# Kernel optimization log

Hardware: AMD Instinct MI355X
Metric: run time of the kernel (lower is better)

Reference implementation:

```python
import jax, jax.numpy as jnp
import numpy as np

EMBED_DIM = 768
N_HEADS = 12
HEAD_DIM = EMBED_DIM // N_HEADS
B, S = 8, 1024


def setup_inputs() -> dict:
    key = jax.random.key(0)
    ks = jax.random.split(key, 7)
    sc = 1.0 / np.sqrt(HEAD_DIM)
    return {
        "sequences": jax.random.normal(ks[0], (B, S, EMBED_DIM), dtype=jnp.float32),
        # per-head Linear weights stored [H, in, out] (torch Linear is x @ W.T + b;
        # with random init the layout convention is equivalent math)
        "Wq": jax.random.normal(ks[1], (N_HEADS, HEAD_DIM, HEAD_DIM), dtype=jnp.float32) * sc,
        "bq": jax.random.normal(ks[2], (N_HEADS, HEAD_DIM), dtype=jnp.float32) * 0.01,
        "Wk": jax.random.normal(ks[3], (N_HEADS, HEAD_DIM, HEAD_DIM), dtype=jnp.float32) * sc,
        "bk": jax.random.normal(ks[4], (N_HEADS, HEAD_DIM), dtype=jnp.float32) * 0.01,
        "Wv": jax.random.normal(ks[5], (N_HEADS, HEAD_DIM, HEAD_DIM), dtype=jnp.float32) * sc,
        "bv": jax.random.normal(ks[6], (N_HEADS, HEAD_DIM), dtype=jnp.float32) * 0.01,
    }


def reference(sequences, Wq, bq, Wk, bk, Wv, bv):
    b, s, d = sequences.shape
    h, hd = Wq.shape[0], Wq.shape[1]
    x = sequences.reshape(b, s, h, hd)              # split embed dim into heads
    q = jnp.einsum("bshd,hde->bshe", x, Wq) + bq    # per-head linear (block-diag GEMM)
    k = jnp.einsum("bshd,hde->bshe", x, Wk) + bk
    v = jnp.einsum("bshd,hde->bshe", x, Wv) + bv
    # NOTE: original module applies NO 1/sqrt(head_dim) scaling
    logits = jnp.einsum("bshe,bthe->bhst", q, k)    # [B,H,S,S]
    attn = jax.nn.softmax(logits, axis=-1)
    out = jnp.einsum("bhst,bthe->bshe", attn, v)    # [B,S,H,hd]
    return out.reshape(b, s, d)
```

## Files before the change

### kernel.cpp

```cpp
#include <hip/hip_runtime.h>
#include <stdint.h>

#define EMBED 768
#define NH 12
#define HD 64
#define Bsz 8
#define Ssz 1024
#define LOG2E 1.44269504088896f

typedef __attribute__((ext_vector_type(4))) float f32x4;
typedef __attribute__((ext_vector_type(8))) _Float16 f16x8;
typedef __attribute__((ext_vector_type(4))) _Float16 f16x4;
typedef __attribute__((ext_vector_type(2))) _Float16 f16x2;

__device__ __forceinline__ int SW(int row, int col) {
    return row * 64 + (col ^ ((row & 7) << 3));
}

__launch_bounds__(256)
__global__ void qkv_proj(const float* __restrict__ x,
                         const float* __restrict__ Wq, const float* __restrict__ bq,
                         const float* __restrict__ Wk, const float* __restrict__ bk,
                         const float* __restrict__ Wv, const float* __restrict__ bv,
                         _Float16* __restrict__ Qb, _Float16* __restrict__ Kb,
                         _Float16* __restrict__ Vt)
{
    __shared__ _Float16 XT[128 * 72];
    __shared__ _Float16 Wt[3 * 64 * 72];
    __shared__ float Bs[192];

    const int bt = blockIdx.x;
    const int st = bt & 7;
    const int h  = (bt >> 3) % NH;
    const int b  = bt / (8 * NH);
    const int sbase = st * 128;
    const int tid = threadIdx.x;
    const int lane = tid & 63, w = tid >> 6;
    const int l15 = lane & 15, quad = lane >> 4;

    for (int i = 0; i < 8; ++i) {
        int idx = tid + 256 * i;
        int row = idx >> 4;
        int c4  = (idx & 15) * 4;
        const float4 g = *(const float4*)&x[(size_t)(b * Ssz + sbase + row) * EMBED + h * HD + c4];
        f16x4 v; v[0] = (_Float16)g.x; v[1] = (_Float16)g.y; v[2] = (_Float16)g.z; v[3] = (_Float16)g.w;
        *(f16x4*)&XT[row * 72 + c4] = v;
    }
    {
        const float* Ws0[3] = {Wq, Wk, Wv};
        const float* bs0[3] = {bq, bk, bv};
#pragma unroll
        for (int m = 0; m < 3; ++m) {
            const float* W = Ws0[m] + (size_t)h * HD * HD;
            for (int i = 0; i < 4; ++i) {
                int idx = tid + 256 * i;
                int d = idx >> 4, e4 = (idx & 15) * 4;
                float4 g = *(const float4*)&W[d * 64 + e4];
                Wt[m * 4608 + (e4 + 0) * 72 + d] = (_Float16)g.x;
                Wt[m * 4608 + (e4 + 1) * 72 + d] = (_Float16)g.y;
                Wt[m * 4608 + (e4 + 2) * 72 + d] = (_Float16)g.z;
                Wt[m * 4608 + (e4 + 3) * 72 + d] = (_Float16)g.w;
            }
        }
        if (tid < 192) Bs[tid] = bs0[tid >> 6][h * HD + (tid & 63)];
    }
    __syncthreads();

    f16x8 bx[2][2];
    const int nbg0 = w * 2;
#pragma unroll
    for (int nb = 0; nb < 2; ++nb)
#pragma unroll
        for (int kh = 0; kh < 2; ++kh)
            bx[nb][kh] = *(const f16x8*)&XT[((nbg0 + nb) * 16 + l15) * 72 + kh * 32 + quad * 8];
    __syncthreads();

    const size_t qkbase = (size_t)(b * NH + h) * Ssz + sbase;
    const f32x4 zero = {0.f, 0.f, 0.f, 0.f};

#pragma unroll
    for (int m = 0; m < 3; ++m) {
        f32x4 acc[2][4];
#pragma unroll
        for (int nb = 0; nb < 2; ++nb)
#pragma unroll
            for (int eb = 0; eb < 4; ++eb) acc[nb][eb] = zero;
#pragma unroll
        for (int eb = 0; eb < 4; ++eb)
#pragma unroll
            for (int kh = 0; kh < 2; ++kh) {
                f16x8 aw = *(const f16x8*)&Wt[m * 4608 + (eb * 16 + l15) * 72 + kh * 32 + quad * 8];
#pragma unroll
                for (int nb = 0; nb < 2; ++nb)
                    acc[nb][eb] = __builtin_amdgcn_mfma_f32_16x16x32_f16(aw, bx[nb][kh], acc[nb][eb], 0, 0, 0);
            }

        if (m < 2) {
            const float sc = (m == 0) ? LOG2E : 1.0f;
#pragma unroll
            for (int nb = 0; nb < 2; ++nb)
#pragma unroll
                for (int eb = 0; eb < 4; ++eb) {
                    f32x4 bb = *(const f32x4*)&Bs[m * 64 + eb * 16 + quad * 4];
                    f16x4 v;
#pragma unroll
                    for (int r = 0; r < 4; ++r) v[r] = (_Float16)((acc[nb][eb][r] + bb[r]) * sc);
                    *(f16x4*)&XT[((nbg0 + nb) * 16 + l15) * 72 + eb * 16 + quad * 4] = v;
                }
            __syncthreads();
            _Float16* outp = (m == 0) ? Qb : Kb;
            for (int i = 0; i < 4; ++i) {
                int idx = tid + 256 * i;
                int s = idx >> 3, e8 = (idx & 7) * 8;
                *(f16x8*)&outp[(qkbase + s) * HD + e8] = *(const f16x8*)&XT[s * 72 + e8];
            }
            __syncthreads();
        } else {
            _Float16* Vs = XT;
#pragma unroll
            for (int nb = 0; nb < 2; ++nb)
#pragma unroll
                for (int eb = 0; eb < 4; ++eb) {
                    f32x4 bb = *(const f32x4*)&Bs[128 + eb * 16 + quad * 4];
#pragma unroll
                    for (int r = 0; r < 4; ++r)
                        Vs[(eb * 16 + quad * 4 + r) * 136 + (nbg0 + nb) * 16 + l15] =
                            (_Float16)(acc[nb][eb][r] + bb[r]);
                }
            __syncthreads();
            for (int i = 0; i < 4; ++i) {
                int idx = tid + 256 * i;
                int e = idx >> 4, s8 = (idx & 15) * 8;
                *(f16x8*)&Vt[((size_t)(b * NH + h) * 64 + e) * Ssz + sbase + s8] =
                    *(const f16x8*)&Vs[e * 136 + s8];
            }
        }
    }
}

#define KVBUF 9216
__launch_bounds__(512)
__global__ void attn(const _Float16* __restrict__ Qb, const _Float16* __restrict__ Kb,
                     const _Float16* __restrict__ Vt, float* __restrict__ out)
{
    __shared__ _Float16 KV[2 * KVBUF];
    __shared__ _Float16 Pl[8 * 16 * 64];

    const int bt = blockIdx.x;
    const int hh = bt % 96;
    const int qt = bt / 96;
    const int h  = hh % NH;
    const int b  = hh / NH;

    const int tid = threadIdx.x;
    const int lane = tid & 63, w = tid >> 6;
    const int l15 = lane & 15, quad = lane >> 4;

    const size_t bh = (size_t)(b * NH + h);
    const _Float16* Qg = Qb + bh * Ssz * HD;
    const _Float16* Kg = Kb + bh * Ssz * HD;
    const _Float16* Vg = Vt + bh * (size_t)HD * Ssz;

    const int qrow0 = qt * 128 + w * 16;
    f16x8 aq[2];
#pragma unroll
    for (int kh = 0; kh < 2; ++kh)
        aq[kh] = *(const f16x8*)&Qg[(qrow0 + l15) * HD + kh * 32 + quad * 8];

    const f32x4 zero = {0.f, 0.f, 0.f, 0.f};
    f32x4 o[5];
#pragma unroll
    for (int eb = 0; eb < 5; ++eb) o[eb] = zero;
    float m_run = -INFINITY;

    const int srow = tid >> 3;
    const int scol = (tid & 7) * 8;
    const int swst = SW(srow, scol);

    {
        int bufi = tid >> 8;
        int r16  = (tid >> 4) & 15;
        int c4   = (tid & 15) * 4;
        f16x4 v;
        _Float16 val = (r16 == 0) ? (_Float16)1.0f : (_Float16)0.0f;
        v[0] = val; v[1] = val; v[2] = val; v[3] = val;
        *(f16x4*)&KV[bufi * KVBUF + 4096 + SW(64 + r16, c4)] = v;
    }

    f16x8 kr = *(const f16x8*)&Kg[srow * HD + scol];
    f16x8 vr = *(const f16x8*)&Vg[(size_t)srow * Ssz + scol];
    *(f16x8*)&KV[swst] = kr;
    *(f16x8*)&KV[4096 + swst] = vr;
    __syncthreads();

    _Float16* Pw = &Pl[w * 1024];
    const int swq = (l15 & 7) << 3;

    for (int kt = 0; kt < 16; ++kt) {
        const int cur = kt & 1;
        if (kt < 15) {
            kr = *(const f16x8*)&Kg[((kt + 1) * 64 + srow) * HD + scol];
            vr = *(const f16x8*)&Vg[(size_t)srow * Ssz + (kt + 1) * 64 + scol];
        }
        const _Float16* Ksb = &KV[cur * KVBUF];
        const _Float16* Vsb = &KV[cur * KVBUF + 4096];

        f32x4 st[4];
#pragma unroll
        for (int tb = 0; tb < 4; ++tb) {
            f32x4 acc = zero;
#pragma unroll
            for (int kh = 0; kh < 2; ++kh) {
                f16x8 ak = *(const f16x8*)&Ksb[SW(tb * 16 + l15, kh * 32 + quad * 8)];
                acc = __builtin_amdgcn_mfma_f32_16x16x32_f16(ak, aq[kh], acc, 0, 0, 0);
            }
            st[tb] = acc;
        }

        float mt = st[0][0];
#pragma unroll
        for (int tb = 0; tb < 4; ++tb)
#pragma unroll
            for (int r = 0; r < 4; ++r) mt = fmaxf(mt, st[tb][r]);
        mt = fmaxf(mt, __shfl_xor(mt, 16, 64));
        mt = fmaxf(mt, __shfl_xor(mt, 32, 64));
        float mn = fmaxf(m_run, mt);
        float al = __builtin_amdgcn_exp2f(m_run - mn);
        m_run = mn;
        f16x4 pv[4];
#pragma unroll
        for (int tb = 0; tb < 4; ++tb) {
            float p0 = __builtin_amdgcn_exp2f(st[tb][0] - mn);
            float p1 = __builtin_amdgcn_exp2f(st[tb][1] - mn);
            float p2 = __builtin_amdgcn_exp2f(st[tb][2] - mn);
            float p3 = __builtin_amdgcn_exp2f(st[tb][3] - mn);
            f16x2 lo = __builtin_bit_cast(f16x2, __builtin_amdgcn_cvt_pkrtz(p0, p1));
            f16x2 hi = __builtin_bit_cast(f16x2, __builtin_amdgcn_cvt_pkrtz(p2, p3));
            pv[tb][0] = lo[0]; pv[tb][1] = lo[1]; pv[tb][2] = hi[0]; pv[tb][3] = hi[1];
        }

#pragma unroll
        for (int tb = 0; tb < 4; ++tb)
            *(f16x4*)&Pw[l15 * 64 + ((tb * 16 + quad * 4) ^ swq)] = pv[tb];

        if (kt < 15) {
            const int nxt = cur ^ 1;
            *(f16x8*)&KV[nxt * KVBUF + swst] = kr;
            *(f16x8*)&KV[nxt * KVBUF + 4096 + swst] = vr;
        }
        __asm__ __volatile__("s_waitcnt lgkmcnt(0)" ::: "memory");
        f16x8 bp[2];
#pragma unroll
        for (int kh = 0; kh < 2; ++kh)
            bp[kh] = *(const f16x8*)&Pw[l15 * 64 + ((kh * 32 + quad * 8) ^ swq)];

#pragma unroll
        for (int eb = 0; eb < 5; ++eb) o[eb] *= al;

#pragma unroll
        for (int kh = 0; kh < 2; ++kh)
#pragma unroll
            for (int eb = 0; eb < 5; ++eb) {
                f16x8 av = *(const f16x8*)&Vsb[SW(eb * 16 + l15, kh * 32 + quad * 8)];
                o[eb] = __builtin_amdgcn_mfma_f32_16x16x32_f16(av, bp[kh], o[eb], 0, 0, 0);
            }

        __syncthreads();
    }

    const float lv = __shfl(o[4][0], l15, 64);
    const float inv = 1.f / lv;
    const int q = qrow0 + l15;
    float* op = &out[(size_t)(b * Ssz + q) * EMBED + h * HD + quad * 4];
#pragma unroll
    for (int eb = 0; eb < 4; ++eb) {
        f32x4 r = o[eb] * inv;
        *(f32x4*)&op[eb * 16] = r;
    }
}

extern "C" void kernel_launch(void* const* d_in, const int* in_sizes, int n_in,
                              void* d_out, int out_size, void* d_ws, size_t ws_size,
                              hipStream_t stream) {
    const float* x  = (const float*)d_in[0];
    const float* Wq = (const float*)d_in[1];
    const float* bq = (const float*)d_in[2];
    const float* Wk = (const float*)d_in[3];
    const float* bk = (const float*)d_in[4];
    const float* Wv = (const float*)d_in[5];
    const float* bv = (const float*)d_in[6];

    _Float16* Qb = (_Float16*)d_ws;
    _Float16* Kb = Qb + (size_t)Bsz * NH * Ssz * HD;
    _Float16* Vt = Kb + (size_t)Bsz * NH * Ssz * HD;

    qkv_proj<<<dim3(Bsz * NH * 8), dim3(256), 0, stream>>>(x, Wq, bq, Wk, bk, Wv, bv, Qb, Kb, Vt);
    attn<<<dim3(Bsz * NH * 8), dim3(512), 0, stream>>>(Qb, Kb, Vt, (float*)d_out);
}
```

Baseline: 135.9 us.

## Restructure attention kernel around 32x32 MFMA with register-resident P and async LDS loads

Rewrites the attention kernel to use 32x32x16 MFMA tiles with 4 waves of 32 query rows each instead of 8 waves of 16 rows. The P tile now stays in registers, rearranged with cross-lane shuffles, instead of round-tripping through LDS. K/V tiles are staged with global_load_lds direct-to-LDS copies using pre-swizzled source addresses. The row sum is tracked explicitly instead of through the ones-row trick, rescaling is skipped unless the max grows by more than a threshold, and setprio hints wrap the MFMA sections. Fewer threads per block and the lazy rescale carry occupancy and numerical-range risks.

```diff
diff --git a/kernel.cpp b/kernel.cpp
--- a/kernel.cpp
+++ b/kernel.cpp
@@ -9,13 +9,11 @@
 #define LOG2E 1.44269504088896f
 
 typedef __attribute__((ext_vector_type(4))) float f32x4;
+typedef __attribute__((ext_vector_type(16))) float f32x16;
 typedef __attribute__((ext_vector_type(8))) _Float16 f16x8;
 typedef __attribute__((ext_vector_type(4))) _Float16 f16x4;
 typedef __attribute__((ext_vector_type(2))) _Float16 f16x2;
-
-__device__ __forceinline__ int SW(int row, int col) {
-    return row * 64 + (col ^ ((row & 7) << 3));
-}
+typedef __attribute__((ext_vector_type(4))) unsigned int u32x4;
 
 __launch_bounds__(256)
 __global__ void qkv_proj(const float* __restrict__ x,
@@ -138,13 +136,12 @@
     }
 }
 
-#define KVBUF 9216
-__launch_bounds__(512)
+#define KVB 8192
+__launch_bounds__(256)
 __global__ void attn(const _Float16* __restrict__ Qb, const _Float16* __restrict__ Kb,
                      const _Float16* __restrict__ Vt, float* __restrict__ out)
 {
-    __shared__ _Float16 KV[2 * KVBUF];
-    __shared__ _Float16 Pl[8 * 16 * 64];
+    __shared__ _Float16 KV[2 * KVB];
 
     const int bt = blockIdx.x;
     const int hh = bt % 96;
@@ -152,131 +149,157 @@
     const int h  = hh % NH;
     const int b  = hh / NH;
 
-    const int tid = threadIdx.x;
+    const int tid  = threadIdx.x;
     const int lane = tid & 63, w = tid >> 6;
-    const int l15 = lane & 15, quad = lane >> 4;
+    const int l31  = lane & 31;
+    const int hf   = lane >> 5;
+    const bool hi  = (hf != 0);
 
     const size_t bh = (size_t)(b * NH + h);
     const _Float16* Qg = Qb + bh * Ssz * HD;
     const _Float16* Kg = Kb + bh * Ssz * HD;
     const _Float16* Vg = Vt + bh * (size_t)HD * Ssz;
 
-    const int qrow0 = qt * 128 + w * 16;
-    f16x8 aq[2];
-#pragma unroll
-    for (int kh = 0; kh < 2; ++kh)
-        aq[kh] = *(const f16x8*)&Qg[(qrow0 + l15) * HD + kh * 32 + quad * 8];
-
-    const f32x4 zero = {0.f, 0.f, 0.f, 0.f};
-    f32x4 o[5];
-#pragma unroll
-    for (int eb = 0; eb < 5; ++eb) o[eb] = zero;
-    float m_run = -INFINITY;
-
-    const int srow = tid >> 3;
-    const int scol = (tid & 7) * 8;
-    const int swst = SW(srow, scol);
-
-    {
-        int bufi = tid >> 8;
-        int r16  = (tid >> 4) & 15;
-        int c4   = (tid & 15) * 4;
-        f16x4 v;
-        _Float16 val = (r16 == 0) ? (_Float16)1.0f : (_Float16)0.0f;
-        v[0] = val; v[1] = val; v[2] = val; v[3] = val;
-        *(f16x4*)&KV[bufi * KVBUF + 4096 + SW(64 + r16, c4)] = v;
-    }
-
-    f16x8 kr = *(const f16x8*)&Kg[srow * HD + scol];
-    f16x8 vr = *(const f16x8*)&Vg[(size_t)srow * Ssz + scol];
-    *(f16x8*)&KV[swst] = kr;
-    *(f16x8*)&KV[4096 + swst] = vr;
+    const int qrow = qt * 128 + w * 32 + l31;
+    f16x8 aq[4];
+#pragma unroll
+    for (int kk = 0; kk < 4; ++kk)
+        aq[kk] = *(const f16x8*)&Qg[(size_t)qrow * HD + kk * 16 + hf * 8];
+
+    const int ca = tid, cb = tid + 256;
+    const int ra = ca >> 3, ga = (ca & 7) ^ (ra & 7);
+    const int rb = cb >> 3, gb = (cb & 7) ^ (rb & 7);
+    const _Float16* Ka  = Kg + ra * HD + ga * 8;
+    const _Float16* Kb2 = Kg + rb * HD + gb * 8;
+    const _Float16* Va  = Vg + (size_t)ra * Ssz + ga * 8;
+    const _Float16* Vb  = Vg + (size_t)rb * Ssz + gb * 8;
+
+#define STAGE(buf, kt_) do {                                                            \
+    __builtin_amdgcn_global_load_lds(                                                   \
+        (const __attribute__((address_space(1))) void*)(Ka + (kt_) * 64 * HD),          \
+        (__attribute__((address_space(3))) void*)&KV[(buf) * KVB + ca * 8], 16, 0, 0);  \
+    __builtin_amdgcn_global_load_lds(                                                   \
+        (const __attribute__((address_space(1))) void*)(Kb2 + (kt_) * 64 * HD),         \
+        (__attribute__((address_space(3))) void*)&KV[(buf) * KVB + cb * 8], 16, 0, 0);  \
+    __builtin_amdgcn_global_load_lds(                                                   \
+        (const __attribute__((address_space(1))) void*)(Va + (kt_) * 64),               \
+        (__attribute__((address_space(3))) void*)&KV[(buf) * KVB + 4096 + ca * 8], 16, 0, 0); \
+    __builtin_amdgcn_global_load_lds(                                                   \
+        (const __attribute__((address_space(1))) void*)(Vb + (kt_) * 64),               \
+        (__attribute__((address_space(3))) void*)&KV[(buf) * KVB + 4096 + cb * 8], 16, 0, 0); \
+} while (0)
+
+    STAGE(0, 0);
+
+    f32x16 o0, o1;
+#pragma unroll
+    for (int i = 0; i < 16; ++i) { o0[i] = 0.f; o1[i] = 0.f; }
+    float m_run = -INFINITY, l_run = 0.f;
+
+    const int rsw = l31 * 64;
+    const int sx  = (l31 & 7) << 3;
+    const int ch  = hf * 8;
+
+    __asm__ __volatile__("s_waitcnt vmcnt(0)" ::: "memory");
     __syncthreads();
-
-    _Float16* Pw = &Pl[w * 1024];
-    const int swq = (l15 & 7) << 3;
 
     for (int kt = 0; kt < 16; ++kt) {
         const int cur = kt & 1;
-        if (kt < 15) {
-            kr = *(const f16x8*)&Kg[((kt + 1) * 64 + srow) * HD + scol];
-            vr = *(const f16x8*)&Vg[(size_t)srow * Ssz + (kt + 1) * 64 + scol];
-        }
-        const _Float16* Ksb = &KV[cur * KVBUF];
-        const _Float16* Vsb = &KV[cur * KVBUF + 4096];
-
-        f32x4 st[4];
-#pragma unroll
-        for (int tb = 0; tb < 4; ++tb) {
-            f32x4 acc = zero;
-#pragma unroll
-            for (int kh = 0; kh < 2; ++kh) {
-                f16x8 ak = *(const f16x8*)&Ksb[SW(tb * 16 + l15, kh * 32 + quad * 8)];
-                acc = __builtin_amdgcn_mfma_f32_16x16x32_f16(ak, aq[kh], acc, 0, 0, 0);
-            }
-            st[tb] = acc;
-        }
-
-        float mt = st[0][0];
-#pragma unroll
-        for (int tb = 0; tb < 4; ++tb)
-#pragma unroll
-            for (int r = 0; r < 4; ++r) mt = fmaxf(mt, st[tb][r]);
-        mt = fmaxf(mt, __shfl_xor(mt, 16, 64));
+        if (kt < 15) STAGE(cur ^ 1, kt + 1);
+
+        const _Float16* Ksb = &KV[cur * KVB];
+        const _Float16* Vsb = &KV[cur * KVB + 4096];
+
+        f32x16 st0, st1;
+#pragma unroll
+        for (int i = 0; i < 16; ++i) { st0[i] = 0.f; st1[i] = 0.f; }
+        __builtin_amdgcn_s_setprio(1);
+#pragma unroll
+        for (int kk = 0; kk < 4; ++kk) {
+            const int col = (kk * 16 + ch) ^ sx;
+            f16x8 ak0 = *(const f16x8*)&Ksb[rsw + col];
+            f16x8 ak1 = *(const f16x8*)&Ksb[2048 + rsw + col];
+            st0 = __builtin_amdgcn_mfma_f32_32x32x16_f16(ak0, aq[kk], st0, 0, 0, 0);
+            st1 = __builtin_amdgcn_mfma_f32_32x32x16_f16(ak1, aq[kk], st1, 0, 0, 0);
+        }
+        __builtin_amdgcn_s_setprio(0);
+
+        float mt = st0[0];
+#pragma unroll
+        for (int i = 1; i < 16; ++i) mt = fmaxf(mt, st0[i]);
+#pragma unroll
+        for (int i = 0; i < 16; ++i) mt = fmaxf(mt, st1[i]);
         mt = fmaxf(mt, __shfl_xor(mt, 32, 64));
-        float mn = fmaxf(m_run, mt);
-        float al = __builtin_amdgcn_exp2f(m_run - mn);
-        m_run = mn;
-        f16x4 pv[4];
-#pragma unroll
-        for (int tb = 0; tb < 4; ++tb) {
-            float p0 = __builtin_amdgcn_exp2f(st[tb][0] - mn);
-            float p1 = __builtin_amdgcn_exp2f(st[tb][1] - mn);
-            float p2 = __builtin_amdgcn_exp2f(st[tb][2] - mn);
-            float p3 = __builtin_amdgcn_exp2f(st[tb][3] - mn);
-            f16x2 lo = __builtin_bit_cast(f16x2, __builtin_amdgcn_cvt_pkrtz(p0, p1));
-            f16x2 hi = __builtin_bit_cast(f16x2, __builtin_amdgcn_cvt_pkrtz(p2, p3));
-            pv[tb][0] = lo[0]; pv[tb][1] = lo[1]; pv[tb][2] = hi[0]; pv[tb][3] = hi[1];
-        }
-
-#pragma unroll
-        for (int tb = 0; tb < 4; ++tb)
-            *(f16x4*)&Pw[l15 * 64 + ((tb * 16 + quad * 4) ^ swq)] = pv[tb];
-
-        if (kt < 15) {
-            const int nxt = cur ^ 1;
-            *(f16x8*)&KV[nxt * KVBUF + swst] = kr;
-            *(f16x8*)&KV[nxt * KVBUF + 4096 + swst] = vr;
-        }
-        __asm__ __volatile__("s_waitcnt lgkmcnt(0)" ::: "memory");
-        f16x8 bp[2];
-#pragma unroll
-        for (int kh = 0; kh < 2; ++kh)
-            bp[kh] = *(const f16x8*)&Pw[l15 * 64 + ((kh * 32 + quad * 8) ^ swq)];
-
-#pragma unroll
-        for (int eb = 0; eb < 5; ++eb) o[eb] *= al;
-
-#pragma unroll
-        for (int kh = 0; kh < 2; ++kh)
-#pragma unroll
-            for (int eb = 0; eb < 5; ++eb) {
-                f16x8 av = *(const f16x8*)&Vsb[SW(eb * 16 + l15, kh * 32 + quad * 8)];
-                o[eb] = __builtin_amdgcn_mfma_f32_16x16x32_f16(av, bp[kh], o[eb], 0, 0, 0);
-            }
-
+
+        if (__any(mt > m_run + 8.f)) {
+            float mn = fmaxf(m_run, mt);
+            float al = __builtin_amdgcn_exp2f(m_run - mn);
+            m_run = mn;
+            l_run *= al;
+#pragma unroll
+            for (int i = 0; i < 16; ++i) { o0[i] *= al; o1[i] *= al; }
+        }
+
+#pragma unroll
+        for (int i = 0; i < 16; ++i) st0[i] = __builtin_amdgcn_exp2f(st0[i] - m_run);
+#pragma unroll
+        for (int i = 0; i < 16; ++i) st1[i] = __builtin_amdgcn_exp2f(st1[i] - m_run);
+
+        float a0 = 0.f, a1 = 0.f, a2 = 0.f, a3 = 0.f;
+#pragma unroll
+        for (int i = 0; i < 16; i += 4) {
+            a0 += st0[i]; a1 += st0[i+1]; a2 += st0[i+2]; a3 += st0[i+3];
+            a0 += st1[i]; a1 += st1[i+1]; a2 += st1[i+2]; a3 += st1[i+3];
+        }
+        float ls = (a0 + a1) + (a2 + a3);
+        ls += __shfl_xor(ls, 32, 64);
+        l_run += ls;
+
+        __builtin_amdgcn_s_setprio(1);
+#pragma unroll
+        for (int kk = 0; kk < 4; ++kk) {
+            const f32x16& pp = (kk < 2) ? st0 : st1;
+            const int rb8 = 8 * (kk & 1);
+            unsigned x0 = __builtin_bit_cast(unsigned, __builtin_amdgcn_cvt_pkrtz(pp[rb8+0], pp[rb8+1]));
+            unsigned y0 = __builtin_bit_cast(unsigned, __builtin_amdgcn_cvt_pkrtz(pp[rb8+4], pp[rb8+5]));
+            unsigned x1 = __builtin_bit_cast(unsigned, __builtin_amdgcn_cvt_pkrtz(pp[rb8+2], pp[rb8+3]));
+            unsigned y1 = __builtin_bit_cast(unsigned, __builtin_amdgcn_cvt_pkrtz(pp[rb8+6], pp[rb8+7]));
+            unsigned x0o = (unsigned)__shfl_xor((int)x0, 32, 64);
+            unsigned y0o = (unsigned)__shfl_xor((int)y0, 32, 64);
+            unsigned x1o = (unsigned)__shfl_xor((int)x1, 32, 64);
+            unsigned y1o = (unsigned)__shfl_xor((int)y1, 32, 64);
+            unsigned d0 = hi ? y0o : x0;
+            unsigned d1 = hi ? y1o : x1;
+            unsigned d2 = hi ? y0  : x0o;
+            unsigned d3 = hi ? y1  : x1o;
+            u32x4 du = {d0, d1, d2, d3};
+            f16x8 bp = __builtin_bit_cast(f16x8, du);
+            const int col = (kk * 16 + ch) ^ sx;
+            f16x8 av0 = *(const f16x8*)&Vsb[rsw + col];
+            f16x8 av1 = *(const f16x8*)&Vsb[2048 + rsw + col];
+            o0 = __builtin_amdgcn_mfma_f32_32x32x16_f16(av0, bp, o0, 0, 0, 0);
+            o1 = __builtin_amdgcn_mfma_f32_32x32x16_f16(av1, bp, o1, 0, 0, 0);
+        }
+        __builtin_amdgcn_s_setprio(0);
+
+        __asm__ __volatile__("s_waitcnt vmcnt(0)" ::: "memory");
         __syncthreads();
     }
 
-    const float lv = __shfl(o[4][0], l15, 64);
-    const float inv = 1.f / lv;
-    const int q = qrow0 + l15;
-    float* op = &out[(size_t)(b * Ssz + q) * EMBED + h * HD + quad * 4];
-#pragma unroll
-    for (int eb = 0; eb < 4; ++eb) {
-        f32x4 r = o[eb] * inv;
-        *(f32x4*)&op[eb * 16] = r;
-    }
+    const float inv = 1.f / l_run;
+    float* op = &out[((size_t)b * Ssz + qrow) * EMBED + h * HD];
+#pragma unroll
+    for (int r1 = 0; r1 < 4; ++r1) {
+        f32x4 v0, v1;
+#pragma unroll
+        for (int r0 = 0; r0 < 4; ++r0) {
+            v0[r0] = o0[4 * r1 + r0] * inv;
+            v1[r0] = o1[4 * r1 + r0] * inv;
+        }
+        *(f32x4*)&op[r1 * 8 + hf * 4]      = v0;
+        *(f32x4*)&op[32 + r1 * 8 + hf * 4] = v1;
+    }
+#undef STAGE
 }
 
 extern "C" void kernel_launch(void* const* d_in, const int* in_sizes, int n_in,
@@ -295,5 +318,5 @@
     _Float16* Vt = Kb + (size_t)Bsz * NH * Ssz * HD;
 
     qkv_proj<<<dim3(Bsz * NH * 8), dim3(256), 0, stream>>>(x, Wq, bq, Wk, bk, Wv, bv, Qb, Kb, Vt);
-    attn<<<dim3(Bsz * NH * 8), dim3(512), 0, stream>>>(Qb, Kb, Vt, (float*)d_out);
+    attn<<<dim3(Bsz * NH * 8), dim3(256), 0, stream>>>(Qb, Kb, Vt, (float*)d_out);
 }
```

Result: no change. 138.6 us (+1.9%).
